# Optimization experiments

Hardware: AMD Instinct MI355X
Metric: run time of the kernel (lower is better)

Reference implementation:

```python
import jax, jax.numpy as jnp
import numpy as np
from jax import lax

B, N, D = 8, 4096, 768
H, K, U, V = 12, 16, 4, 64   # heads, key_depth, intra_depth, lambda_query_size
L = 23                        # local_context_size (odd)
PAD = L // 2
EPS = 1e-5


def setup_inputs() -> dict:
    key = jax.random.key(0)
    ks = jax.random.split(key, 9)
    return {
        "x": jax.random.normal(ks[0], (B, N, D), dtype=jnp.float32),
        "Wq": jax.random.normal(ks[1], (H * K, D), dtype=jnp.float32) * 0.02,
        "Wk": jax.random.normal(ks[2], (K * U, D), dtype=jnp.float32) * 0.02,
        "Wv": jax.random.normal(ks[3], (V * U, D), dtype=jnp.float32) * 0.02,
        "gamma_q": 1.0 + 0.1 * jax.random.normal(ks[4], (H * K,), dtype=jnp.float32),
        "beta_q": 0.1 * jax.random.normal(ks[5], (H * K,), dtype=jnp.float32),
        "gamma_v": 1.0 + 0.1 * jax.random.normal(ks[6], (V * U,), dtype=jnp.float32),
        "beta_v": 0.1 * jax.random.normal(ks[7], (V * U,), dtype=jnp.float32),
        "rel_pos_embed": jax.random.normal(ks[8], (K, U, 1, L), dtype=jnp.float32),
    }


def _batchnorm1d(z, gamma, beta):
    # z: (b, c, n); training-mode BatchNorm1d (biased variance over batch+length)
    mean = jnp.mean(z, axis=(0, 2), keepdims=True)
    var = jnp.mean((z - mean) ** 2, axis=(0, 2), keepdims=True)
    zhat = (z - mean) * lax.rsqrt(var + EPS)
    return zhat * gamma[None, :, None] + beta[None, :, None]


def reference(x, Wq, Wk, Wv, gamma_q, beta_q, gamma_v, beta_v, rel_pos_embed):
    b, n, d = x.shape
    xT = jnp.swapaxes(x, 1, 2)                      # b d n
    q = jnp.einsum('od,bdn->bon', Wq, xT)           # b (h k) n
    k = jnp.einsum('od,bdn->bon', Wk, xT)           # b (k u) n
    v = jnp.einsum('od,bdn->bon', Wv, xT)           # b (v u) n
    q = _batchnorm1d(q, gamma_q, beta_q)
    v = _batchnorm1d(v, gamma_v, beta_v)
    q = q.reshape(b, H, K, n)                       # b h k n
    k = k.reshape(b, K, U, n).transpose(0, 2, 1, 3) # b u k n
    v = v.reshape(b, V, U, n).transpose(0, 2, 1, 3) # b u v n
    k = jax.nn.softmax(k, axis=-1)                  # softmax over positions
    lam_c = jnp.einsum('bukn,buvn->bkv', k, v)      # content lambda
    Yc = jnp.einsum('bhkn,bkv->bnhv', q, lam_c)
    # position lambda via local conv over positions: v (b,u,V,n) * W (K,u,1,L) -> (b,K,V,n)
    lam_p = lax.conv_general_dilated(
        v, rel_pos_embed, window_strides=(1, 1),
        padding=((0, 0), (PAD, PAD)),
        dimension_numbers=('NCHW', 'OIHW', 'NCHW'))
    Yp = jnp.einsum('bhkn,bkvn->bnhv', q, lam_p)
    Y = (Yc + Yp).reshape(b, n, H * V)
    return Y
```

## Files before the change

### kernel.cpp

```cpp
#include <hip/hip_runtime.h>
#include <hip/hip_bf16.h>

constexpr int B = 8, N = 4096, D = 768;
constexpr int H = 12, K = 16, U = 4, V = 64, L = 23, PAD = 11;
constexpr int CQ = 192;
constexpr int CK = 64;
constexpr int CV = 256;
constexpr int CT = 512;
constexpr int CV0 = CQ + CK;
constexpr float EPS = 1e-5f;

typedef _Float16 f16x8 __attribute__((ext_vector_type(8)));
typedef _Float16 f16x4 __attribute__((ext_vector_type(4)));
typedef _Float16 f16x2 __attribute__((ext_vector_type(2)));
typedef float    f32x4 __attribute__((ext_vector_type(4)));

#define GLOAD16(gp, lp) __builtin_amdgcn_global_load_lds( \
    (const __attribute__((address_space(1))) void*)(gp),  \
    (__attribute__((address_space(3))) void*)(lp), 16, 0, 0)

__device__ __forceinline__ f16x2 pkrtz(float a, float b) {
    return __builtin_bit_cast(f16x2, __builtin_amdgcn_cvt_pkrtz(a, b));
}

__device__ __forceinline__ f16x8 cvt8r(float4 a, float4 b) {
    f16x8 r;
    r[0] = (_Float16)a.x; r[1] = (_Float16)a.y; r[2] = (_Float16)a.z; r[3] = (_Float16)a.w;
    r[4] = (_Float16)b.x; r[5] = (_Float16)b.y; r[6] = (_Float16)b.z; r[7] = (_Float16)b.w;
    return r;
}

__global__ __launch_bounds__(256) void k_w16(
    const float* __restrict__ Wq, const float* __restrict__ Wk,
    const float* __restrict__ Wv, const float* __restrict__ rel,
    _Float16* __restrict__ Wh, _Float16* __restrict__ relSg)
{
    const int bid = blockIdx.x;
    const int tid = threadIdx.x;
    if (bid < 192) {
        const int idx = bid * 256 + tid;
        const int c = idx / 96, g = idx % 96;
        const float* src;
        if (c < CQ)       src = Wq + (size_t)c * D;
        else if (c < CV0) src = Wk + (size_t)(c - CQ) * D;
        else              src = Wv + (size_t)(c - CV0) * D;
        float4 a = *(const float4*)(src + g * 8);
        float4 b = *(const float4*)(src + g * 8 + 4);
        *(f16x8*)(Wh + (size_t)c * D + g * 8) = cvt8r(a, b);
    } else {
        const int base = ((bid - 192) * 256 + tid) * 8;
        f16x8 o;
        #pragma unroll
        for (int j = 0; j < 8; ++j) {
            const int e = base + j;
            const int jj = e & 31, kk = (e >> 5) & 15;
            const int uu = (e >> 9) & 3, dd = e >> 11;
            const int l = jj - dd;
            float v = (l >= 0 && l < L) ? rel[(kk * U + uu) * L + l] : 0.f;
            o[j] = (_Float16)v;
        }
        *(f16x8*)(relSg + base) = o;
    }
}

__global__ __launch_bounds__(512) void k_proj(
    const float* __restrict__ x, const _Float16* __restrict__ Wh,
    _Float16* __restrict__ Ph)
{
    __shared__ _Float16 As0[256 * 32], As1[256 * 32], As2[256 * 32];
    __shared__ float    Bs0[256 * 32], Bs1[256 * 32], Bs2[256 * 32];
    const int b  = blockIdx.z;
    const int bc = blockIdx.y * 256;
    const int bn = blockIdx.x * 256;
    const int tid  = threadIdx.x;
    const int lane = tid & 63;
    const int wave = tid >> 6;
    const int wr  = wave >> 2;
    const int wcn = wave & 3;
    const int fr = lane & 15, sl = lane >> 4;

    const int arow_l = lane >> 2;
    const int achk   = (lane & 3) ^ (arow_l & 3) ^ ((arow_l >> 2) & 3);
    const int brow_l = lane >> 3;
    const int bchk   = (lane & 7) ^ brow_l;

    const _Float16* Wbase = Wh + (size_t)bc * D;
    const float*    xbase = x + ((size_t)b * N + bn) * D;

    const int ca = sl ^ (fr & 3) ^ ((fr >> 2) & 3);
    const int mb = fr & 7;

    f32x4 acc[8][4] = {};

#define STAGE(Ap, Bp, kt) do {                                         \
        _Pragma("unroll")                                              \
        for (int j = 0; j < 2; ++j) {                                  \
            const int r0 = wave * 32 + j * 16;                         \
            GLOAD16(Wbase + (size_t)(r0 + arow_l) * D + (kt) + achk * 8, \
                    (Ap) + r0 * 32);                                   \
        }                                                              \
        _Pragma("unroll")                                              \
        for (int j = 0; j < 4; ++j) {                                  \
            const int r0 = wave * 32 + j * 8;                          \
            GLOAD16(xbase + (size_t)(r0 + brow_l) * D + (kt) + bchk * 4, \
                    (Bp) + r0 * 32);                                   \
        }                                                              \
    } while (0)

#define WAIT6  asm volatile("s_waitcnt vmcnt(6)" ::: "memory")
#define WAIT0  asm volatile("s_waitcnt vmcnt(0)" ::: "memory")
#define BAR    __builtin_amdgcn_s_barrier()
#define SCHED0 __builtin_amdgcn_sched_barrier(0)

#define PHASE(Ap, Bp, StageStmt, WaitStmt) do {                        \
        f16x8 af[8]; float4 pa[4], pb[4];                              \
        _Pragma("unroll")                                              \
        for (int mi = 0; mi < 8; ++mi) {                               \
            const int ra = wr * 128 + mi * 16 + fr;                    \
            af[mi] = *(const f16x8*)((Ap) + ra * 32 + ca * 8);         \
        }                                                              \
        _Pragma("unroll")                                              \
        for (int ni = 0; ni < 4; ++ni) {                               \
            const int rb = wcn * 64 + ni * 16 + fr;                    \
            pa[ni] = *(const float4*)((Bp) + rb * 32 + (((sl * 2) ^ mb) * 4)); \
            pb[ni] = *(const float4*)((Bp) + rb * 32 + (((sl * 2 + 1) ^ mb) * 4)); \
        }                                                              \
        StageStmt;                                                     \
        WaitStmt;                                                      \
        SCHED0; BAR;                                                   \
        f16x8 bfr[4];                                                  \
        _Pragma("unroll")                                              \
        for (int ni = 0; ni < 4; ++ni) {                               \
            f16x2 p0 = pkrtz(pa[ni].x, pa[ni].y);                      \
            f16x2 p1 = pkrtz(pa[ni].z, pa[ni].w);                      \
            f16x2 p2 = pkrtz(pb[ni].x, pb[ni].y);                      \
            f16x2 p3 = pkrtz(pb[ni].z, pb[ni].w);                      \
            f16x8 bv;                                                  \
            bv[0] = p0[0]; bv[1] = p0[1]; bv[2] = p1[0]; bv[3] = p1[1]; \
            bv[4] = p2[0]; bv[5] = p2[1]; bv[6] = p3[0]; bv[7] = p3[1]; \
            bfr[ni] = bv;                                              \
        }                                                              \
        __builtin_amdgcn_s_setprio(1);                                 \
        _Pragma("unroll")                                              \
        for (int mi = 0; mi < 8; ++mi)                                 \
            _Pragma("unroll")                                          \
            for (int ni = 0; ni < 4; ++ni)                             \
                acc[mi][ni] = __builtin_amdgcn_mfma_f32_16x16x32_f16(  \
                    af[mi], bfr[ni], acc[mi][ni], 0, 0, 0);            \
        __builtin_amdgcn_s_setprio(0);                                 \
        SCHED0; BAR;                                                   \
    } while (0)

    STAGE(As0, Bs0, 0);
    STAGE(As1, Bs1, 32);
    WAIT6;
    BAR;

    for (int t0 = 0; t0 < 21; t0 += 3) {
        const int kt = t0 * 32;
        PHASE(As0, Bs0, STAGE(As2, Bs2, kt + 64),  WAIT6);
        PHASE(As1, Bs1, STAGE(As0, Bs0, kt + 96),  WAIT6);
        PHASE(As2, Bs2, STAGE(As1, Bs1, kt + 128), WAIT6);
    }
    PHASE(As0, Bs0, STAGE(As2, Bs2, 736), WAIT6);
    PHASE(As1, Bs1, (void)0, WAIT0);
    PHASE(As2, Bs2, (void)0, (void)0);

#undef STAGE
#undef PHASE
#undef WAIT6
#undef WAIT0
#undef BAR
#undef SCHED0

    _Float16* Pb = Ph + ((size_t)b * CT + bc) * N + bn;
    #pragma unroll
    for (int mi = 0; mi < 8; ++mi)
        #pragma unroll
        for (int ni = 0; ni < 4; ++ni)
            #pragma unroll
            for (int r = 0; r < 4; ++r) {
                const int row = wr * 128 + mi * 16 + sl * 4 + r;
                const int col = wcn * 64 + ni * 16 + fr;
                Pb[(size_t)row * N + col] = (_Float16)acc[mi][ni][r];
            }
}

__global__ __launch_bounds__(256) void k_stats(
    const _Float16* __restrict__ Ph,
    const float* __restrict__ gq, const float* __restrict__ bq,
    const float* __restrict__ gv, const float* __restrict__ bv,
    float* __restrict__ sArr, float* __restrict__ tArr,
    float* __restrict__ mxk, float* __restrict__ invk,
    float* __restrict__ lamC)
{
    const int bid = blockIdx.x;
    const int tid = threadIdx.x;

    if (bid < CQ + CV) {
        const int ci = bid;
        const int c  = (ci < CQ) ? ci : ci + CK;
        float g, be;
        if (ci < CQ) { g = gq[ci];      be = bq[ci]; }
        else         { g = gv[ci - CQ]; be = bv[ci - CQ]; }

        float s = 0.f, s2 = 0.f;
        for (int b = 0; b < B; ++b) {
            const _Float16* row = Ph + ((size_t)b * CT + c) * N;
            #pragma unroll
            for (int i = 0; i < 2; ++i) {
                f16x8 v = ((const f16x8*)row)[i * 256 + tid];
                #pragma unroll
                for (int j = 0; j < 8; ++j) {
                    float f = (float)v[j];
                    s += f; s2 += f * f;
                }
            }
        }
        #pragma unroll
        for (int off = 32; off; off >>= 1) {
            s  += __shfl_xor(s, off);
            s2 += __shfl_xor(s2, off);
        }
        __shared__ float ls[4], ls2[4];
        if ((tid & 63) == 0) { ls[tid >> 6] = s; ls2[tid >> 6] = s2; }
        __syncthreads();
        if (tid == 0) {
            float S = ls[0] + ls[1] + ls[2] + ls[3];
            float S2 = ls2[0] + ls2[1] + ls2[2] + ls2[3];
            const float invM = 1.0f / (float)(B * N);
            float mean = S * invM;
            float var  = S2 * invM - mean * mean;
            float sc   = g / sqrtf(var + EPS);
            sArr[c] = sc;
            tArr[c] = be - mean * sc;
        }
    } else {
        const int idx = bid - (CQ + CV);
        if (idx < 8) {
            ((float4*)lamC)[idx * 256 + tid] = float4{0.f, 0.f, 0.f, 0.f};
        }
        const int b = idx >> 6, kc = idx & 63;
        const _Float16* row = Ph + ((size_t)b * CT + CQ + kc) * N;
        float v[16];
        float m = -3.4e38f;
        #pragma unroll
        for (int i = 0; i < 2; ++i) {
            f16x8 t = ((const f16x8*)row)[i * 256 + tid];
            #pragma unroll
            for (int j = 0; j < 8; ++j) {
                v[i*8+j] = (float)t[j];
                m = fmaxf(m, v[i*8+j]);
            }
        }
        #pragma unroll
        for (int off = 32; off; off >>= 1) m = fmaxf(m, __shfl_xor(m, off));
        __shared__ float rA[4], rB[4];
        if ((tid & 63) == 0) rA[tid >> 6] = m;
        __syncthreads();
        m = fmaxf(fmaxf(rA[0], rA[1]), fmaxf(rA[2], rA[3]));
        float s = 0.f;
        #pragma unroll
        for (int i = 0; i < 16; ++i) s += __expf(v[i] - m);
        #pragma unroll
        for (int off = 32; off; off >>= 1) s += __shfl_xor(s, off);
        if ((tid & 63) == 0) rB[tid >> 6] = s;
        __syncthreads();
        if (tid == 0) {
            s = rB[0] + rB[1] + rB[2] + rB[3];
            mxk[b * CK + kc]  = m;
            invk[b * CK + kc] = 1.f / s;
        }
    }
}

__global__ __launch_bounds__(256) void k_mid(
    const _Float16* __restrict__ Ph, const float* __restrict__ mxk,
    const float* __restrict__ invk, const float* __restrict__ sArr,
    const float* __restrict__ tArr, float* __restrict__ lamC,
    _Float16* __restrict__ qT)
{
    __shared__ float smem[128 * 20 + 128 * 67];
    const int bid = blockIdx.x;
    const int tid = threadIdx.x;

    if (bid < 256) {
        float (*Kt)[20] = (float(*)[20])smem;
        float (*Vt)[67] = (float(*)[67])(smem + 128 * 20);
        const int cx = bid & 7, u = (bid >> 3) & 3, b = bid >> 5;
        const int chunk0 = cx * 512;
        const int vv = tid & 63, kg = tid >> 6;
        float acc[4] = {0.f, 0.f, 0.f, 0.f};

        const int kk = tid >> 4, sK = tid & 15;
        const float mm = mxk[b * CK + kk * U + u];
        const float iv = invk[b * CK + kk * U + u];

        for (int sc = 0; sc < 4; ++sc) {
            const int nbase = chunk0 + sc * 128;
            __syncthreads();
            {
                f16x8 v = *(const f16x8*)(Ph + ((size_t)b * CT + CQ + kk * U + u) * N
                                          + nbase + sK * 8);
                #pragma unroll
                for (int i = 0; i < 8; ++i)
                    Kt[sK * 8 + i][kk] = __expf((float)v[i] - mm) * iv;
            }
            {
                #pragma unroll
                for (int it = 0; it < 4; ++it) {
                    const int task = it * 256 + tid;
                    const int vvv = task >> 4, sV = task & 15;
                    const int c = CV0 + vvv * U + u;
                    f16x8 v = *(const f16x8*)(Ph + ((size_t)b * CT + c) * N
                                              + nbase + sV * 8);
                    const float sc2 = sArr[c], tt = tArr[c];
                    #pragma unroll
                    for (int i = 0; i < 8; ++i)
                        Vt[sV * 8 + i][vvv] = (float)v[i] * sc2 + tt;
                }
            }
            __syncthreads();
            #pragma unroll 4
            for (int n = 0; n < 128; ++n) {
                float4 kv = *(const float4*)&Kt[n][kg * 4];
                float vx = Vt[n][vv];
                acc[0] += kv.x * vx; acc[1] += kv.y * vx;
                acc[2] += kv.z * vx; acc[3] += kv.w * vx;
            }
        }
        #pragma unroll
        for (int j = 0; j < 4; ++j)
            atomicAdd(&lamC[((size_t)b * K + kg * 4 + j) * V + vv], acc[j]);
    } else {
        _Float16 (*tl)[40] = (_Float16(*)[40])smem;
        const int q  = bid - 256;
        const int n0 = (q & 63) * 64;
        const int c0 = ((q >> 6) % 6) * 32;
        const int b  = q / 384;

        const int ch = tid >> 3, seg = tid & 7;
        const int c = c0 + ch;
        f16x8 v = *(const f16x8*)(Ph + ((size_t)b * CT + c) * N + n0 + seg * 8);
        const float sc = sArr[c], tt = tArr[c];
        #pragma unroll
        for (int i = 0; i < 8; ++i)
            tl[seg * 8 + i][ch] = (_Float16)((float)v[i] * sc + tt);
        __syncthreads();

        const int n = tid >> 2, part = tid & 3;
        f16x8 o = *(const f16x8*)&tl[n][part * 8];
        *(f16x8*)(qT + ((size_t)b * N + n0 + n) * CQ + c0 + part * 8) = o;
    }
}

__global__ __launch_bounds__(512, 4) void k_out(
    const _Float16* __restrict__ Ph, const _Float16* __restrict__ relSg,
    const float* __restrict__ lamC, const float* __restrict__ sArr,
    const float* __restrict__ tArr, const _Float16* __restrict__ qT,
    float* __restrict__ Y)
{
    constexpr int NT = 32;
    constexpr int VST = 72;
    __shared__ _Float16 vsegT[256 * VST];

    const int b  = blockIdx.y;
    const int n0 = blockIdx.x * NT;
    const int tid  = threadIdx.x;
    const int lane = tid & 63;
    const int wave = tid >> 6;
    const int fr = lane & 15;
    const int sl = lane >> 4;

    #pragma unroll
    for (int it = 0; it < 4; ++it) {
        const int task = it * 512 + tid;
        const int ch = task >> 3, s = task & 7;
        const int c = CV0 + ch;
        const int row = (ch & 3) * 64 + (ch >> 2);
        const int nbase = n0 - 16 + s * 8;
        const float sc = sArr[c], tt = tArr[c];
        const bool full = (nbase >= 0) && (nbase + 8 <= N);
        f16x8 v{};
        if (full)
            v = *(const f16x8*)(Ph + ((size_t)b * CT + c) * N + nbase);
        #pragma unroll
        for (int i = 0; i < 8; ++i) {
            const int np = s * 8 - 5 + i;
            if (np < 0 || np >= 56) continue;
            float val = 0.f;
            if (full) {
                val = (float)v[i] * sc + tt;
            } else {
                const int n = nbase + i;
                if (n >= 0 && n < N)
                    val = (float)Ph[((size_t)b * CT + c) * N + n] * sc + tt;
            }
            vsegT[row * VST + np] = (_Float16)val;
        }
    }
    const int vg = wave & 3;
    const int nb = (wave >> 2) * 16;
    float lc[4];
    #pragma unroll
    for (int r = 0; r < 4; ++r)
        lc[r] = lamC[(size_t)b * K * V + (sl * 4 + r) * V + vg * 16 + fr];
    __syncthreads();

    const _Float16* qTb = qT + (size_t)b * N * CQ;

    for (int dlt = 0; dlt < 8; ++dlt) {
        f16x8 aU[4];
        #pragma unroll
        for (int u = 0; u < 4; ++u)
            aU[u] = *(const f16x8*)(relSg + ((dlt * 4 + u) * 16 + fr) * 32 + sl * 8);
        #pragma unroll
        for (int rep = 0; rep < 2; ++rep) {
            const int A  = nb + rep * 8;
            const int nn = A + dlt;
            f32x4 acc = {lc[0], lc[1], lc[2], lc[3]};
            #pragma unroll
            for (int u = 0; u < 4; ++u) {
                f16x8 bf = *(const f16x8*)(vsegT + (u * 64 + vg * 16 + fr) * VST + A + sl * 8);
                acc = __builtin_amdgcn_mfma_f32_16x16x32_f16(aU[u], bf, acc, 0, 0, 0);
            }
            f16x4 lam16;
            #pragma unroll
            for (int r = 0; r < 4; ++r) lam16[r] = (_Float16)acc[r];
            f16x4 q4 = *(const f16x4*)(qTb + (size_t)(n0 + nn) * CQ + fr * 16 + sl * 4);
            f32x4 y = {0.f, 0.f, 0.f, 0.f};
            y = __builtin_amdgcn_mfma_f32_16x16x16f16(q4, lam16, y, 0, 0, 0);
            if (sl < 3) {
                float* yr = Y + ((size_t)b * N + n0 + nn) * (H * V) + vg * 16 + fr;
                #pragma unroll
                for (int r = 0; r < 4; ++r)
                    yr[(sl * 4 + r) * 64] = y[r];
            }
        }
    }
}

extern "C" void kernel_launch(void* const* d_in, const int* in_sizes, int n_in,
                              void* d_out, int out_size, void* d_ws, size_t ws_size,
                              hipStream_t stream)
{
    const float* x   = (const float*)d_in[0];
    const float* Wq  = (const float*)d_in[1];
    const float* Wk  = (const float*)d_in[2];
    const float* Wv  = (const float*)d_in[3];
    const float* gq  = (const float*)d_in[4];
    const float* bq  = (const float*)d_in[5];
    const float* gv  = (const float*)d_in[6];
    const float* bv  = (const float*)d_in[7];
    const float* rel = (const float*)d_in[8];
    float* Y = (float*)d_out;

    _Float16* Ph  = (_Float16*)d_ws;
    float* sArr = (float*)(Ph + (size_t)B * CT * N);
    float* tArr = sArr + CT;
    float* lamC = tArr + CT;
    float* mxk  = lamC + (size_t)B * K * V;
    float* invk = mxk + B * CK;
    _Float16* qT = (_Float16*)(invk + B * CK);
    _Float16* Wh = qT + (size_t)B * N * CQ;
    _Float16* relSg = Wh + (size_t)CT * D;

    k_w16  <<<dim3(192 + 8), 256, 0, stream>>>(Wq, Wk, Wv, rel, Wh, relSg);
    k_proj <<<dim3(N / 256, CT / 256, B), 512, 0, stream>>>(x, Wh, Ph);
    k_stats<<<dim3(CQ + CV + B * CK), 256, 0, stream>>>(Ph, gq, bq, gv, bv,
                                                        sArr, tArr, mxk, invk, lamC);
    k_mid  <<<dim3(256 + 3072), 256, 0, stream>>>(Ph, mxk, invk, sArr, tArr, lamC, qT);
    k_out  <<<dim3(N / 32, B), 512, 0, stream>>>(Ph, relSg, lamC, sArr, tArr, qT, Y);
}
```

Measured before the change: 114.7 us.

## Shrink projection GEMM tile and convert x to fp16 in registers before LDS

The projection GEMM now uses a 256x128 output tile instead of 256x256, and a two-stage LDS double buffer instead of three stages. The x operand is loaded into registers, converted to fp16, and written to LDS, so LDS holds only fp16 and each wave no longer converts its B fragments every phase. Smaller LDS use and launch_bounds(512,4) aim to fit more blocks per CU and launch twice as many blocks. The cost is a synchronous vmcnt(0) wait on each stage, less reuse of W per tile, and the A fragments are now read from LDS inside the MFMA loop.

```diff
diff --git a/kernel.cpp b/kernel.cpp
--- a/kernel.cpp
+++ b/kernel.cpp
@@ -63,15 +63,15 @@
     }
 }
 
-__global__ __launch_bounds__(512) void k_proj(
+__global__ __launch_bounds__(512, 4) void k_proj(
     const float* __restrict__ x, const _Float16* __restrict__ Wh,
     _Float16* __restrict__ Ph)
 {
-    __shared__ _Float16 As0[256 * 32], As1[256 * 32], As2[256 * 32];
-    __shared__ float    Bs0[256 * 32], Bs1[256 * 32], Bs2[256 * 32];
+    __shared__ _Float16 As0[256 * 32], As1[256 * 32];
+    __shared__ _Float16 Bs0[128 * 32], Bs1[128 * 32];
     const int b  = blockIdx.z;
     const int bc = blockIdx.y * 256;
-    const int bn = blockIdx.x * 256;
+    const int bn = blockIdx.x * 128;
     const int tid  = threadIdx.x;
     const int lane = tid & 63;
     const int wave = tid >> 6;
@@ -81,95 +81,80 @@
 
     const int arow_l = lane >> 2;
     const int achk   = (lane & 3) ^ (arow_l & 3) ^ ((arow_l >> 2) & 3);
-    const int brow_l = lane >> 3;
-    const int bchk   = (lane & 7) ^ brow_l;
+    const int ca = sl ^ (fr & 3) ^ ((fr >> 2) & 3);
 
     const _Float16* Wbase = Wh + (size_t)bc * D;
-    const float*    xbase = x + ((size_t)b * N + bn) * D;
-
-    const int ca = sl ^ (fr & 3) ^ ((fr >> 2) & 3);
-    const int mb = fr & 7;
-
-    f32x4 acc[8][4] = {};
-
-#define STAGE(Ap, Bp, kt) do {                                         \
+
+    const int brow = tid >> 2;
+    const int bq   = tid & 3;
+    const int bqs  = bq ^ (brow & 3) ^ ((brow >> 2) & 3);
+    const float* xrow = x + ((size_t)b * N + bn + brow) * D + bq * 8;
+    _Float16* const bdst0 = Bs0 + brow * 32 + bqs * 8;
+    _Float16* const bdst1 = Bs1 + brow * 32 + bqs * 8;
+
+    f32x4 acc[8][2] = {};
+
+#define STAGE_A(Ap, kt) do {                                           \
         _Pragma("unroll")                                              \
         for (int j = 0; j < 2; ++j) {                                  \
             const int r0 = wave * 32 + j * 16;                         \
             GLOAD16(Wbase + (size_t)(r0 + arow_l) * D + (kt) + achk * 8, \
                     (Ap) + r0 * 32);                                   \
         }                                                              \
-        _Pragma("unroll")                                              \
-        for (int j = 0; j < 4; ++j) {                                  \
-            const int r0 = wave * 32 + j * 8;                          \
-            GLOAD16(xbase + (size_t)(r0 + brow_l) * D + (kt) + bchk * 4, \
-                    (Bp) + r0 * 32);                                   \
-        }                                                              \
     } while (0)
 
-#define WAIT6  asm volatile("s_waitcnt vmcnt(6)" ::: "memory")
 #define WAIT0  asm volatile("s_waitcnt vmcnt(0)" ::: "memory")
+#define LGKM0  asm volatile("s_waitcnt lgkmcnt(0)" ::: "memory")
 #define BAR    __builtin_amdgcn_s_barrier()
 #define SCHED0 __builtin_amdgcn_sched_barrier(0)
 
-#define PHASE(Ap, Bp, StageStmt, WaitStmt) do {                        \
-        f16x8 af[8]; float4 pa[4], pb[4];                              \
-        _Pragma("unroll")                                              \
-        for (int mi = 0; mi < 8; ++mi) {                               \
-            const int ra = wr * 128 + mi * 16 + fr;                    \
-            af[mi] = *(const f16x8*)((Ap) + ra * 32 + ca * 8);         \
-        }                                                              \
-        _Pragma("unroll")                                              \
-        for (int ni = 0; ni < 4; ++ni) {                               \
-            const int rb = wcn * 64 + ni * 16 + fr;                    \
-            pa[ni] = *(const float4*)((Bp) + rb * 32 + (((sl * 2) ^ mb) * 4)); \
-            pb[ni] = *(const float4*)((Bp) + rb * 32 + (((sl * 2 + 1) ^ mb) * 4)); \
-        }                                                              \
-        StageStmt;                                                     \
-        WaitStmt;                                                      \
-        SCHED0; BAR;                                                   \
-        f16x8 bfr[4];                                                  \
-        _Pragma("unroll")                                              \
-        for (int ni = 0; ni < 4; ++ni) {                               \
-            f16x2 p0 = pkrtz(pa[ni].x, pa[ni].y);                      \
-            f16x2 p1 = pkrtz(pa[ni].z, pa[ni].w);                      \
-            f16x2 p2 = pkrtz(pb[ni].x, pb[ni].y);                      \
-            f16x2 p3 = pkrtz(pb[ni].z, pb[ni].w);                      \
-            f16x8 bv;                                                  \
-            bv[0] = p0[0]; bv[1] = p0[1]; bv[2] = p1[0]; bv[3] = p1[1]; \
-            bv[4] = p2[0]; bv[5] = p2[1]; bv[6] = p3[0]; bv[7] = p3[1]; \
-            bfr[ni] = bv;                                              \
+#define PHASE(Acur, Bcur, Anxt, Bnxt, Bdnxt, ktn, STAGEON) do {        \
+        f16x8 bf0 = *(const f16x8*)((Bcur) + (wcn * 32 + fr) * 32 + ca * 8);       \
+        f16x8 bf1 = *(const f16x8*)((Bcur) + (wcn * 32 + 16 + fr) * 32 + ca * 8);  \
+        float4 xr0{}, xr1{};                                           \
+        if (STAGEON) {                                                 \
+            STAGE_A(Anxt, ktn);                                        \
+            xr0 = *(const float4*)(xrow + (ktn));                      \
+            xr1 = *(const float4*)(xrow + (ktn) + 4);                  \
         }                                                              \
         __builtin_amdgcn_s_setprio(1);                                 \
         _Pragma("unroll")                                              \
-        for (int mi = 0; mi < 8; ++mi)                                 \
-            _Pragma("unroll")                                          \
-            for (int ni = 0; ni < 4; ++ni)                             \
-                acc[mi][ni] = __builtin_amdgcn_mfma_f32_16x16x32_f16(  \
-                    af[mi], bfr[ni], acc[mi][ni], 0, 0, 0);            \
+        for (int mi = 0; mi < 8; ++mi) {                               \
+            f16x8 af = *(const f16x8*)((Acur) + (wr * 128 + mi * 16 + fr) * 32 + ca * 8); \
+            acc[mi][0] = __builtin_amdgcn_mfma_f32_16x16x32_f16(af, bf0, acc[mi][0], 0, 0, 0); \
+            acc[mi][1] = __builtin_amdgcn_mfma_f32_16x16x32_f16(af, bf1, acc[mi][1], 0, 0, 0); \
+        }                                                              \
         __builtin_amdgcn_s_setprio(0);                                 \
-        SCHED0; BAR;                                                   \
+        if (STAGEON) {                                                 \
+            WAIT0;                                                     \
+            *(f16x8*)(Bdnxt) = cvt8r(xr0, xr1);                        \
+            LGKM0; SCHED0;                                             \
+        }                                                              \
+        BAR;                                                           \
     } while (0)
 
-    STAGE(As0, Bs0, 0);
-    STAGE(As1, Bs1, 32);
-    WAIT6;
+    STAGE_A(As0, 0);
+    {
+        float4 p0 = *(const float4*)(xrow);
+        float4 p1 = *(const float4*)(xrow + 4);
+        WAIT0;
+        *(f16x8*)(bdst0) = cvt8r(p0, p1);
+        LGKM0; SCHED0;
+    }
     BAR;
 
-    for (int t0 = 0; t0 < 21; t0 += 3) {
-        const int kt = t0 * 32;
-        PHASE(As0, Bs0, STAGE(As2, Bs2, kt + 64),  WAIT6);
-        PHASE(As1, Bs1, STAGE(As0, Bs0, kt + 96),  WAIT6);
-        PHASE(As2, Bs2, STAGE(As1, Bs1, kt + 128), WAIT6);
-    }
-    PHASE(As0, Bs0, STAGE(As2, Bs2, 736), WAIT6);
-    PHASE(As1, Bs1, (void)0, WAIT0);
-    PHASE(As2, Bs2, (void)0, (void)0);
-
-#undef STAGE
+    for (int kt = 0; kt < D; kt += 64) {
+        PHASE(As0, Bs0, As1, Bs1, bdst1, kt + 32, true);
+        if (kt + 64 < D) {
+            PHASE(As1, Bs1, As0, Bs0, bdst0, kt + 64, true);
+        } else {
+            PHASE(As1, Bs1, As0, Bs0, bdst0, 0, false);
+        }
+    }
+#undef STAGE_A
 #undef PHASE
-#undef WAIT6
 #undef WAIT0
+#undef LGKM0
 #undef BAR
 #undef SCHED0
 
@@ -177,11 +162,11 @@
     #pragma unroll
     for (int mi = 0; mi < 8; ++mi)
         #pragma unroll
-        for (int ni = 0; ni < 4; ++ni)
+        for (int ni = 0; ni < 2; ++ni)
             #pragma unroll
             for (int r = 0; r < 4; ++r) {
                 const int row = wr * 128 + mi * 16 + sl * 4 + r;
-                const int col = wcn * 64 + ni * 16 + fr;
+                const int col = wcn * 32 + ni * 16 + fr;
                 Pb[(size_t)row * N + col] = (_Float16)acc[mi][ni][r];
             }
 }
@@ -466,7 +451,7 @@
     _Float16* relSg = Wh + (size_t)CT * D;
 
     k_w16  <<<dim3(192 + 8), 256, 0, stream>>>(Wq, Wk, Wv, rel, Wh, relSg);
-    k_proj <<<dim3(N / 256, CT / 256, B), 512, 0, stream>>>(x, Wh, Ph);
+    k_proj <<<dim3(N / 128, CT / 256, B), 512, 0, stream>>>(x, Wh, Ph);
     k_stats<<<dim3(CQ + CV + B * CK), 256, 0, stream>>>(Ph, gq, bq, gv, bv,
                                                         sArr, tArr, mxk, invk, lamC);
     k_mid  <<<dim3(256 + 3072), 256, 0, stream>>>(Ph, mxk, invk, sArr, tArr, lamC, qT);
```

New measurement: 281.0 us. 145% more time.
